# Optimization experiments

Measured on AMD Instinct MI355X. Metric: run time of the kernel, lower is better.

## Reference

```python
import jax, jax.numpy as jnp
import numpy as np

EPS = 1e-7  # keras.backend.epsilon()


def setup_inputs() -> dict:
    key = jax.random.key(0)
    kx, kw, ku = jax.random.split(key, 3)
    B, S, F = 16, 4096, 512
    x = jax.random.normal(kx, (B, S, F), dtype=jnp.float32)
    # glorot-uniform-scaled weights
    limW = np.sqrt(6.0 / (F + F)).astype(np.float32)
    W = jax.random.uniform(kw, (F, F), dtype=jnp.float32, minval=-limW, maxval=limW)
    b = jnp.zeros((F,), dtype=jnp.float32)
    limu = np.sqrt(6.0 / (F + 1)).astype(np.float32)
    u = jax.random.uniform(ku, (F,), dtype=jnp.float32, minval=-limu, maxval=limu)
    return {"x": x, "W": W, "b": b, "u": u}


def reference(x, W, b, u):
    # x: [B,S,F]  W: [F,F]  b: [F]  u: [F]
    h = jnp.tanh(jnp.einsum('bsf,fg->bsg', x, W) + b)   # [B,S,F]
    scores = jnp.einsum('bsf,f->bs', h, u)              # [B,S]
    e = jnp.exp(scores)
    # NOTE: faithful to the source, normalization is GLOBAL over all B*S scores
    a = e / (jnp.sum(e) + EPS)                          # [B,S]
    out = jnp.einsum('bsf,bs->bf', x, a)                # [B,F] weighted-sum pool over steps
    return out
```

## Files before the change

### kernel.cpp

```cpp
#include <hip/hip_runtime.h>
#include <stdint.h>

#define EPSV 1e-7f
#define FDIM 512
#define BK 64
#define NROWS 65536

typedef __bf16 bf16_t;
typedef bf16_t bf16x8 __attribute__((ext_vector_type(8)));
typedef unsigned short ushort8 __attribute__((ext_vector_type(8)));
typedef float f32x4 __attribute__((ext_vector_type(4)));

#define AS1 __attribute__((address_space(1)))
#define AS3 __attribute__((address_space(3)))

__device__ __forceinline__ unsigned short f2bf(float f) {
  union { float f; unsigned int u; } c; c.f = f;
  unsigned int u = c.u;
  unsigned int r = u + 0x7fffu + ((u >> 16) & 1u);
  return (unsigned short)(r >> 16);
}
__device__ __forceinline__ float bf2f(unsigned short s) {
  union { unsigned int u; float f; } c; c.u = ((unsigned int)s) << 16;
  return c.f;
}

__device__ __forceinline__ float fast_tanh(float x) {
  x = fminf(15.0f, fmaxf(-15.0f, x));
  float t = __expf(2.0f * x);
  return 1.0f - 2.0f * __builtin_amdgcn_rcpf(t + 1.0f);
}

__global__ __launch_bounds__(256) void convert_fused(
    const float* __restrict__ x, unsigned short* __restrict__ xbf,
    const float* __restrict__ W, unsigned short* __restrict__ Wt,
    float* __restrict__ sumE) {
  __shared__ unsigned short tile[32][34];
  const int t = threadIdx.x;
  if (blockIdx.x < 16384) {
    size_t i = ((size_t)blockIdx.x * 256 + t) * 8;
    float4 lo = *(const float4*)(x + i);
    float4 hi = *(const float4*)(x + i + 4);
    ushort8 v;
    v[0] = f2bf(lo.x); v[1] = f2bf(lo.y); v[2] = f2bf(lo.z); v[3] = f2bf(lo.w);
    v[4] = f2bf(hi.x); v[5] = f2bf(hi.y); v[6] = f2bf(hi.z); v[7] = f2bf(hi.w);
    *(ushort8*)(xbf + i) = v;
  } else {
    const int bi = blockIdx.x - 16384;
    if (bi == 0 && t == 0) *sumE = 0.0f;
    const int tx = t & 31, ty = t >> 5;
    const int bn = bi & 15, bk = bi >> 4;
    const int k0 = bk * 32, n0 = bn * 32;
#pragma unroll
    for (int i = 0; i < 4; ++i) {
      int r = ty + i * 8;
      tile[r][tx] = f2bf(W[(size_t)(k0 + r) * FDIM + n0 + tx]);
    }
    __syncthreads();
#pragma unroll
    for (int i = 0; i < 4; ++i) {
      int r = ty + i * 8;
      Wt[(size_t)(n0 + r) * FDIM + k0 + tx] = tile[tx][r];
    }
  }
}

__global__ __launch_bounds__(256, 4) void gemm_score_st(
    const unsigned short* __restrict__ xbf,
    const unsigned short* __restrict__ Wt,
    const float* __restrict__ bvec, const float* __restrict__ uvec,
    float* __restrict__ spart) {
  __shared__ unsigned short sA[128 * BK];
  __shared__ unsigned short sB[128 * BK];
  __shared__ float score_s[128];
  __shared__ float ub_s[128], bb_s[128];

  const int t = threadIdx.x;
  const int lane = t & 63;
  const int w = t >> 6;
  const int wm = w & 1;
  const int wn = w >> 1;
  const int quad = lane >> 4;
  const int l15 = lane & 15;
  const int nch = blockIdx.x >> 9;
  const int rt = blockIdx.x & 511;
  const int m0 = rt * 128;
  const int col0 = nch * 128;

  if (t < 128) {
    score_s[t] = 0.0f;
    ub_s[t] = uvec[col0 + t];
    bb_s[t] = bvec[col0 + t];
  }

  f32x4 acc[4][4];
#pragma unroll
  for (int mi = 0; mi < 4; ++mi)
#pragma unroll
    for (int ni = 0; ni < 4; ++ni) acc[mi][ni] = (f32x4){0.f, 0.f, 0.f, 0.f};

  for (int kc = 0; kc < FDIM / BK; ++kc) {
    const int kbase = kc * BK;
#pragma unroll
    for (int i = 0; i < 4; ++i) {
      int rb = w * 32 + i * 8;
      int rl = rb + (lane >> 3);
      int j = (lane & 7) ^ (rl & 7);
      const unsigned short* g = xbf + (size_t)(m0 + rl) * FDIM + kbase + j * 8;
      unsigned short* l = (unsigned short*)(sA + rb * 64);
      __builtin_amdgcn_global_load_lds((AS1 void*)(g), (AS3 void*)(l), 16, 0, 0);
    }
#pragma unroll
    for (int i = 0; i < 4; ++i) {
      int nb = w * 32 + i * 8;
      int nl = nb + (lane >> 3);
      int j = (lane & 7) ^ (nl & 7);
      const unsigned short* g = Wt + (size_t)(col0 + nl) * FDIM + kbase + j * 8;
      unsigned short* l = (unsigned short*)(sB + nb * 64);
      __builtin_amdgcn_global_load_lds((AS1 void*)(g), (AS3 void*)(l), 16, 0, 0);
    }
    __syncthreads();
#pragma unroll
    for (int ks = 0; ks < 2; ++ks) {
      bf16x8 af[4], bfr[4];
#pragma unroll
      for (int mi = 0; mi < 4; ++mi) {
        int row = wm * 64 + mi * 16 + l15;
        int phys = (ks * 4 + quad) ^ (row & 7);
        af[mi] = *(const bf16x8*)(const void*)(sA + row * 64 + phys * 8);
      }
#pragma unroll
      for (int ni = 0; ni < 4; ++ni) {
        int row = wn * 64 + ni * 16 + l15;
        int phys = (ks * 4 + quad) ^ (row & 7);
        bfr[ni] = *(const bf16x8*)(const void*)(sB + row * 64 + phys * 8);
      }
#pragma unroll
      for (int mi = 0; mi < 4; ++mi)
#pragma unroll
        for (int ni = 0; ni < 4; ++ni)
          acc[mi][ni] = __builtin_amdgcn_mfma_f32_16x16x32_bf16(
              af[mi], bfr[ni], acc[mi][ni], 0, 0, 0);
    }
    __syncthreads();
  }

  float sc[4][4];
#pragma unroll
  for (int mi = 0; mi < 4; ++mi)
#pragma unroll
    for (int r = 0; r < 4; ++r) sc[mi][r] = 0.0f;
#pragma unroll
  for (int ni = 0; ni < 4; ++ni) {
    int cl = wn * 64 + ni * 16 + l15;
    float uu = ub_s[cl], bb = bb_s[cl];
#pragma unroll
    for (int mi = 0; mi < 4; ++mi)
#pragma unroll
      for (int r = 0; r < 4; ++r)
        sc[mi][r] += uu * fast_tanh(acc[mi][ni][r] + bb);
  }
#pragma unroll
  for (int mi = 0; mi < 4; ++mi)
#pragma unroll
    for (int r = 0; r < 4; ++r) {
      float v = sc[mi][r];
      v += __shfl_xor(v, 1); v += __shfl_xor(v, 2);
      v += __shfl_xor(v, 4); v += __shfl_xor(v, 8);
      if (l15 == 0)
        atomicAdd(&score_s[wm * 64 + mi * 16 + quad * 4 + r], v);
    }
  __syncthreads();
  if (t < 128) spart[(size_t)nch * NROWS + m0 + t] = score_s[t];
}

__global__ __launch_bounds__(256, 8) void pool_score(
    const unsigned short* __restrict__ xbf, const float* __restrict__ spart,
    float* __restrict__ sumE, float* __restrict__ ppool) {
  __shared__ float e_s[32];
  __shared__ float red[4][FDIM];
  const int t = threadIdx.x;
  const int c8 = t & 63, rg = t >> 6;
  const int r0 = blockIdx.x * 32;
  if (t < 32) {
    int i = r0 + t;
    float s = spart[i] + spart[i + NROWS] + spart[i + 2 * NROWS] + spart[i + 3 * NROWS];
    float e = __expf(s);
    e_s[t] = e;
    float v = e;
    v += __shfl_xor(v, 1); v += __shfl_xor(v, 2); v += __shfl_xor(v, 4);
    v += __shfl_xor(v, 8); v += __shfl_xor(v, 16);
    if (t == 0) atomicAdd(sumE, v);
  }
  __syncthreads();
  float a[8];
#pragma unroll
  for (int j = 0; j < 8; ++j) a[j] = 0.0f;
  for (int it = 0; it < 8; ++it) {
    int row = rg * 8 + it;
    ushort8 v = *(const ushort8*)(xbf + (size_t)(r0 + row) * FDIM + c8 * 8);
    float wg = e_s[row];
#pragma unroll
    for (int j = 0; j < 8; ++j) a[j] += bf2f(v[j]) * wg;
  }
  *(float4*)&red[rg][c8 * 8]     = (float4){a[0], a[1], a[2], a[3]};
  *(float4*)&red[rg][c8 * 8 + 4] = (float4){a[4], a[5], a[6], a[7]};
  __syncthreads();
  int c = t, c2 = t + 256;
  float s0 = red[0][c] + red[1][c] + red[2][c] + red[3][c];
  float s1 = red[0][c2] + red[1][c2] + red[2][c2] + red[3][c2];
  ppool[(size_t)blockIdx.x * FDIM + c]  = s0;
  ppool[(size_t)blockIdx.x * FDIM + c2] = s1;
}

__global__ __launch_bounds__(256) void pool_reduce(
    const float* __restrict__ ppool, const float* __restrict__ sumE,
    float* __restrict__ out) {
  const int i = blockIdx.x * 256 + threadIdx.x;
  const int b = i >> 9, f = i & 511;
  float s = 0.0f;
  const float* p = ppool + (size_t)b * 128 * FDIM + f;
  for (int c = 0; c < 128; ++c) s += p[(size_t)c * FDIM];
  out[i] = s / (*sumE + EPSV);
}

__global__ void convert_W_f(const float* __restrict__ W, unsigned short* __restrict__ Wt) {
  __shared__ unsigned short tile[32][34];
  const int t = threadIdx.x;
  const int tx = t & 31, ty = t >> 5;
  const int bn = blockIdx.x & 15, bk = blockIdx.x >> 4;
  const int k0 = bk * 32, n0 = bn * 32;
#pragma unroll
  for (int i = 0; i < 4; ++i) {
    int r = ty + i * 8;
    tile[r][tx] = f2bf(W[(size_t)(k0 + r) * FDIM + n0 + tx]);
  }
  __syncthreads();
#pragma unroll
  for (int i = 0; i < 4; ++i) {
    int r = ty + i * 8;
    Wt[(size_t)(n0 + r) * FDIM + k0 + tx] = tile[tx][r];
  }
}

__global__ __launch_bounds__(256, 4) void gemm_score_f32(
    const float* __restrict__ x, const unsigned short* __restrict__ Wt,
    const float* __restrict__ bvec, const float* __restrict__ uvec,
    float* __restrict__ spart) {
  __shared__ unsigned short sA[128 * BK];
  __shared__ unsigned short sB[128 * BK];
  __shared__ float score_s[128];
  __shared__ float ub_s[128], bb_s[128];
  const int t = threadIdx.x;
  const int lane = t & 63;
  const int w = t >> 6;
  const int wm = w & 1, wn = w >> 1;
  const int quad = lane >> 4, l15 = lane & 15;
  const int nch = blockIdx.x >> 9;
  const int rt = blockIdx.x & 511;
  const int m0 = rt * 128, col0 = nch * 128;
  if (t < 128) { score_s[t] = 0.0f; ub_s[t] = uvec[col0 + t]; bb_s[t] = bvec[col0 + t]; }
  f32x4 acc[4][4];
#pragma unroll
  for (int mi = 0; mi < 4; ++mi)
#pragma unroll
    for (int ni = 0; ni < 4; ++ni) acc[mi][ni] = (f32x4){0.f, 0.f, 0.f, 0.f};
  for (int kc = 0; kc < FDIM / BK; ++kc) {
    const int kbase = kc * BK;
#pragma unroll
    for (int p = 0; p < 4; ++p) {
      int slot = t + 256 * p;
      int row = slot >> 3;
      int j = (slot & 7) ^ (row & 7);
      const float* g = x + (size_t)(m0 + row) * FDIM + kbase + j * 8;
      float4 lo = *(const float4*)g;
      float4 hi = *(const float4*)(g + 4);
      ushort8 v;
      v[0] = f2bf(lo.x); v[1] = f2bf(lo.y); v[2] = f2bf(lo.z); v[3] = f2bf(lo.w);
      v[4] = f2bf(hi.x); v[5] = f2bf(hi.y); v[6] = f2bf(hi.z); v[7] = f2bf(hi.w);
      *(ushort8*)(void*)(sA + slot * 8) = v;
    }
#pragma unroll
    for (int i = 0; i < 4; ++i) {
      int nb = w * 32 + i * 8;
      int nl = nb + (lane >> 3);
      int j = (lane & 7) ^ (nl & 7);
      const unsigned short* g = Wt + (size_t)(col0 + nl) * FDIM + kbase + j * 8;
      unsigned short* l = (unsigned short*)(sB + nb * 64);
      __builtin_amdgcn_global_load_lds((AS1 void*)(g), (AS3 void*)(l), 16, 0, 0);
    }
    __syncthreads();
#pragma unroll
    for (int ks = 0; ks < 2; ++ks) {
      bf16x8 af[4], bfr[4];
#pragma unroll
      for (int mi = 0; mi < 4; ++mi) {
        int row = wm * 64 + mi * 16 + l15;
        int phys = (ks * 4 + quad) ^ (row & 7);
        af[mi] = *(const bf16x8*)(const void*)(sA + row * 64 + phys * 8);
      }
#pragma unroll
      for (int ni = 0; ni < 4; ++ni) {
        int row = wn * 64 + ni * 16 + l15;
        int phys = (ks * 4 + quad) ^ (row & 7);
        bfr[ni] = *(const bf16x8*)(const void*)(sB + row * 64 + phys * 8);
      }
#pragma unroll
      for (int mi = 0; mi < 4; ++mi)
#pragma unroll
        for (int ni = 0; ni < 4; ++ni)
          acc[mi][ni] = __builtin_amdgcn_mfma_f32_16x16x32_bf16(
              af[mi], bfr[ni], acc[mi][ni], 0, 0, 0);
    }
    __syncthreads();
  }
  float sc[4][4];
#pragma unroll
  for (int mi = 0; mi < 4; ++mi)
#pragma unroll
    for (int r = 0; r < 4; ++r) sc[mi][r] = 0.0f;
#pragma unroll
  for (int ni = 0; ni < 4; ++ni) {
    int cl = wn * 64 + ni * 16 + l15;
    float uu = ub_s[cl], bb = bb_s[cl];
#pragma unroll
    for (int mi = 0; mi < 4; ++mi)
#pragma unroll
      for (int r = 0; r < 4; ++r)
        sc[mi][r] += uu * fast_tanh(acc[mi][ni][r] + bb);
  }
#pragma unroll
  for (int mi = 0; mi < 4; ++mi)
#pragma unroll
    for (int r = 0; r < 4; ++r) {
      float v = sc[mi][r];
      v += __shfl_xor(v, 1); v += __shfl_xor(v, 2);
      v += __shfl_xor(v, 4); v += __shfl_xor(v, 8);
      if (l15 == 0)
        atomicAdd(&score_s[wm * 64 + mi * 16 + quad * 4 + r], v);
    }
  __syncthreads();
  if (t < 128) spart[(size_t)nch * NROWS + m0 + t] = score_s[t];
}

__global__ void score_exp(float* __restrict__ spart, float* __restrict__ sumE) {
  __shared__ float ws_[4];
  const int t = threadIdx.x;
  const int i = blockIdx.x * 256 + t;
  float s = spart[i] + spart[i + NROWS] + spart[i + 2 * NROWS] + spart[i + 3 * NROWS];
  float e = __expf(s);
  spart[i] = e;
  float v = e;
  v += __shfl_xor(v, 1);  v += __shfl_xor(v, 2);  v += __shfl_xor(v, 4);
  v += __shfl_xor(v, 8);  v += __shfl_xor(v, 16); v += __shfl_xor(v, 32);
  if ((t & 63) == 0) ws_[t >> 6] = v;
  __syncthreads();
  if (t == 0) atomicAdd(sumE, ws_[0] + ws_[1] + ws_[2] + ws_[3]);
}

__global__ __launch_bounds__(256) void pool_k(
    const float* __restrict__ x, const float* __restrict__ e,
    const float* __restrict__ sumE, float* __restrict__ out) {
  __shared__ float e_s[128];
  __shared__ float4 red[128];
  const int t = threadIdx.x;
  const int b = blockIdx.x >> 5, chunk = blockIdx.x & 31;
  const int g0 = b * 4096 + chunk * 128;
  if (t < 128) e_s[t] = e[g0 + t];
  __syncthreads();
  const int parity = t >> 7, f4 = t & 127;
  float ax = 0.f, ay = 0.f, az = 0.f, aw = 0.f;
  for (int r = 0; r < 64; ++r) {
    int row = r * 2 + parity;
    const float4 xv = *(const float4*)(x + (size_t)(g0 + row) * FDIM + f4 * 4);
    float wgt = e_s[row];
    ax += xv.x * wgt; ay += xv.y * wgt; az += xv.z * wgt; aw += xv.w * wgt;
  }
  if (parity) red[f4] = (float4){ax, ay, az, aw};
  __syncthreads();
  if (!parity) {
    float4 o = red[f4];
    float inv = 1.0f / (*sumE + EPSV);
    float* op = out + (size_t)b * FDIM + f4 * 4;
    atomicAdd(op + 0, (ax + o.x) * inv);
    atomicAdd(op + 1, (ay + o.y) * inv);
    atomicAdd(op + 2, (az + o.z) * inv);
    atomicAdd(op + 3, (aw + o.w) * inv);
  }
}

extern "C" void kernel_launch(void* const* d_in, const int* in_sizes, int n_in,
                              void* d_out, int out_size, void* d_ws, size_t ws_size,
                              hipStream_t stream) {
  (void)in_sizes; (void)n_in;
  const float* x = (const float*)d_in[0];
  const float* W = (const float*)d_in[1];
  const float* b = (const float*)d_in[2];
  const float* u = (const float*)d_in[3];
  float* out = (float*)d_out;

  char* p = (char*)d_ws;
  unsigned short* Wt = (unsigned short*)p;            p += (size_t)FDIM * FDIM * 2;
  float* spart = (float*)p;                           p += (size_t)4 * NROWS * 4;
  float* sumE = (float*)p;                            p += 256;
  float* ppool = (float*)p;                           p += (size_t)2048 * FDIM * 4;
  unsigned short* xbf = (unsigned short*)p;           p += (size_t)NROWS * FDIM * 2;
  const size_t need = (size_t)(p - (char*)d_ws);
  const bool big = ws_size >= need;

  if (big) {
    convert_fused<<<dim3(16384 + 256), dim3(256), 0, stream>>>(x, xbf, W, Wt, sumE);
    gemm_score_st<<<dim3(2048), dim3(256), 0, stream>>>(xbf, Wt, b, u, spart);
    pool_score<<<dim3(2048), dim3(256), 0, stream>>>(xbf, spart, sumE, ppool);
    pool_reduce<<<dim3(32), dim3(256), 0, stream>>>(ppool, sumE, out);
  } else {
    hipMemsetAsync(sumE, 0, sizeof(float), stream);
    hipMemsetAsync(d_out, 0, (size_t)out_size * sizeof(float), stream);
    convert_W_f<<<dim3(256), dim3(256), 0, stream>>>(W, Wt);
    gemm_score_f32<<<dim3(2048), dim3(256), 0, stream>>>(x, Wt, b, u, spart);
    score_exp<<<dim3(NROWS / 256), dim3(256), 0, stream>>>(spart, sumE);
    pool_k<<<dim3(512), dim3(256), 0, stream>>>(x, spart, sumE, out);
  }
}
```

Measured before the change: 284.0 us.

## Fuse score exp and weighted pooling into GEMM tail via last-block counter

Removes the separate pool_score kernel. Each GEMM block increments a per-row-tile atomic counter, and the last of the four column-chunk blocks combines the partial scores, applies exp, adds to the global sum, and pools its 128 rows of bf16 x into a per-tile partial. This saves a kernel launch and a pass that re-reads spart, and it reads x while that tile may still be in cache. In exchange it adds threadfences, an atomic per block, a memset of the counters, and serial tail work on one block in four.

```diff
diff --git a/kernel.cpp b/kernel.cpp
--- a/kernel.cpp
+++ b/kernel.cpp
@@ -23,6 +23,9 @@
 __device__ __forceinline__ float bf2f(unsigned short s) {
   union { unsigned int u; float f; } c; c.u = ((unsigned int)s) << 16;
   return c.f;
+}
+__device__ __forceinline__ float asfloat_u(unsigned int u) {
+  union { unsigned int u; float f; } c; c.u = u; return c.f;
 }
 
 __device__ __forceinline__ float fast_tanh(float x) {
@@ -69,11 +72,14 @@
     const unsigned short* __restrict__ xbf,
     const unsigned short* __restrict__ Wt,
     const float* __restrict__ bvec, const float* __restrict__ uvec,
-    float* __restrict__ spart) {
+    float* __restrict__ spart, unsigned int* __restrict__ cnt,
+    float* __restrict__ sumE, float* __restrict__ ppool) {
   __shared__ unsigned short sA[128 * BK];
   __shared__ unsigned short sB[128 * BK];
   __shared__ float score_s[128];
   __shared__ float ub_s[128], bb_s[128];
+  __shared__ float wsum[2];
+  __shared__ int flag_s;
 
   const int t = threadIdx.x;
   const int lane = t & 63;
@@ -172,45 +178,38 @@
     }
   __syncthreads();
   if (t < 128) spart[(size_t)nch * NROWS + m0 + t] = score_s[t];
-}
-
-__global__ __launch_bounds__(256, 8) void pool_score(
-    const unsigned short* __restrict__ xbf, const float* __restrict__ spart,
-    float* __restrict__ sumE, float* __restrict__ ppool) {
-  __shared__ float e_s[32];
-  __shared__ float red[4][FDIM];
-  const int t = threadIdx.x;
-  const int c8 = t & 63, rg = t >> 6;
-  const int r0 = blockIdx.x * 32;
-  if (t < 32) {
-    int i = r0 + t;
-    float s = spart[i] + spart[i + NROWS] + spart[i + 2 * NROWS] + spart[i + 3 * NROWS];
+
+  __threadfence();
+  __syncthreads();
+  if (t == 0) flag_s = (atomicAdd(&cnt[rt], 1u) == 3u);
+  __syncthreads();
+  if (!flag_s) return;
+  __threadfence();
+
+  if (t < 128) {
+    size_t base = m0 + t;
+    float s = spart[base] + spart[NROWS + base] +
+              spart[2 * NROWS + base] + spart[3 * NROWS + base];
     float e = __expf(s);
-    e_s[t] = e;
+    score_s[t] = e;
     float v = e;
-    v += __shfl_xor(v, 1); v += __shfl_xor(v, 2); v += __shfl_xor(v, 4);
-    v += __shfl_xor(v, 8); v += __shfl_xor(v, 16);
-    if (t == 0) atomicAdd(sumE, v);
-  }
-  __syncthreads();
-  float a[8];
-#pragma unroll
-  for (int j = 0; j < 8; ++j) a[j] = 0.0f;
-  for (int it = 0; it < 8; ++it) {
-    int row = rg * 8 + it;
-    ushort8 v = *(const ushort8*)(xbf + (size_t)(r0 + row) * FDIM + c8 * 8);
-    float wg = e_s[row];
-#pragma unroll
-    for (int j = 0; j < 8; ++j) a[j] += bf2f(v[j]) * wg;
-  }
-  *(float4*)&red[rg][c8 * 8]     = (float4){a[0], a[1], a[2], a[3]};
-  *(float4*)&red[rg][c8 * 8 + 4] = (float4){a[4], a[5], a[6], a[7]};
-  __syncthreads();
-  int c = t, c2 = t + 256;
-  float s0 = red[0][c] + red[1][c] + red[2][c] + red[3][c];
-  float s1 = red[0][c2] + red[1][c2] + red[2][c2] + red[3][c2];
-  ppool[(size_t)blockIdx.x * FDIM + c]  = s0;
-  ppool[(size_t)blockIdx.x * FDIM + c2] = s1;
+    v += __shfl_xor(v, 1);  v += __shfl_xor(v, 2);  v += __shfl_xor(v, 4);
+    v += __shfl_xor(v, 8);  v += __shfl_xor(v, 16); v += __shfl_xor(v, 32);
+    if (lane == 0) wsum[t >> 6] = v;
+  }
+  __syncthreads();
+  if (t == 0) atomicAdd(sumE, wsum[0] + wsum[1]);
+
+  float a0 = 0.f, a1 = 0.f;
+  const unsigned short* xb = xbf + (size_t)m0 * FDIM + t * 2;
+#pragma unroll 8
+  for (int r = 0; r < 128; ++r) {
+    unsigned int pv = *(const unsigned int*)(xb + (size_t)r * FDIM);
+    float wg = score_s[r];
+    a0 += asfloat_u(pv << 16) * wg;
+    a1 += asfloat_u(pv & 0xffff0000u) * wg;
+  }
+  *(float2*)(ppool + (size_t)rt * FDIM + t * 2) = (float2){a0, a1};
 }
 
 __global__ __launch_bounds__(256) void pool_reduce(
@@ -219,8 +218,9 @@
   const int i = blockIdx.x * 256 + threadIdx.x;
   const int b = i >> 9, f = i & 511;
   float s = 0.0f;
-  const float* p = ppool + (size_t)b * 128 * FDIM + f;
-  for (int c = 0; c < 128; ++c) s += p[(size_t)c * FDIM];
+  const float* p = ppool + (size_t)b * 32 * FDIM + f;
+#pragma unroll
+  for (int c = 0; c < 32; ++c) s += p[(size_t)c * FDIM];
   out[i] = s / (*sumE + EPSV);
 }
 
@@ -403,15 +403,17 @@
   unsigned short* Wt = (unsigned short*)p;            p += (size_t)FDIM * FDIM * 2;
   float* spart = (float*)p;                           p += (size_t)4 * NROWS * 4;
   float* sumE = (float*)p;                            p += 256;
-  float* ppool = (float*)p;                           p += (size_t)2048 * FDIM * 4;
+  unsigned int* cnt = (unsigned int*)p;               p += 512 * 4 + 256;
+  float* ppool = (float*)p;                           p += (size_t)512 * FDIM * 4;
   unsigned short* xbf = (unsigned short*)p;           p += (size_t)NROWS * FDIM * 2;
   const size_t need = (size_t)(p - (char*)d_ws);
   const bool big = ws_size >= need;
 
   if (big) {
+    hipMemsetAsync(cnt, 0, 512 * sizeof(unsigned int), stream);
     convert_fused<<<dim3(16384 + 256), dim3(256), 0, stream>>>(x, xbf, W, Wt, sumE);
-    gemm_score_st<<<dim3(2048), dim3(256), 0, stream>>>(xbf, Wt, b, u, spart);
-    pool_score<<<dim3(2048), dim3(256), 0, stream>>>(xbf, spart, sumE, ppool);
+    gemm_score_st<<<dim3(2048), dim3(256), 0, stream>>>(xbf, Wt, b, u, spart,
+                                                        cnt, sumE, ppool);
     pool_reduce<<<dim3(32), dim3(256), 0, stream>>>(ppool, sumE, out);
   } else {
     hipMemsetAsync(sumE, 0, sizeof(float), stream);
```

Measured after the change: 448.7 us. 58.0% more time.

## Double-buffer LDS tiles in bf16 GEMM-score kernel with K=32 stages

Applied to the files above, without the earlier changes.

Replaces the single-buffered K=64 tile loop in the GEMM+score kernel with a two-stage LDS ping-pong of K=32 tiles. The global-to-LDS load for the next stage is issued before computing on the current one, and only one barrier is needed per iteration. This is meant to hide global load latency behind MFMA work. LDS use stays the same, but there are twice as many iterations, each with a single MFMA k-step. The swizzle changes to a 4-way XOR, which may affect bank conflicts. There is also no explicit vmcnt wait before the barrier, so correctness depends on the compiler inserting one.

```diff
diff --git a/kernel.cpp b/kernel.cpp
--- a/kernel.cpp
+++ b/kernel.cpp
@@ -3,7 +3,6 @@
 
 #define EPSV 1e-7f
 #define FDIM 512
-#define BK 64
 #define NROWS 65536
 
 typedef __bf16 bf16_t;
@@ -65,13 +64,13 @@
   }
 }
 
-__global__ __launch_bounds__(256, 4) void gemm_score_st(
+__global__ __launch_bounds__(256, 4) void gemm_score_db(
     const unsigned short* __restrict__ xbf,
     const unsigned short* __restrict__ Wt,
     const float* __restrict__ bvec, const float* __restrict__ uvec,
     float* __restrict__ spart) {
-  __shared__ unsigned short sA[128 * BK];
-  __shared__ unsigned short sB[128 * BK];
+  __shared__ unsigned short sA[2][128 * 32];
+  __shared__ unsigned short sB[2][128 * 32];
   __shared__ float score_s[128];
   __shared__ float ub_s[128], bb_s[128];
 
@@ -93,57 +92,62 @@
     bb_s[t] = bvec[col0 + t];
   }
 
+  const unsigned short* abase = xbf + (size_t)m0 * FDIM;
+  const unsigned short* bbase = Wt + (size_t)col0 * FDIM;
+
+#define STAGE2(SRC, SMEM, KC, BUF)                                          \
+  {                                                                         \
+    const int kbase_ = (KC)*32;                                             \
+    _Pragma("unroll") for (int i_ = 0; i_ < 2; ++i_) {                      \
+      int idx_ = w * 2 + i_;                                                \
+      int slot_ = idx_ * 64 + lane;                                         \
+      int r_ = slot_ >> 2;                                                  \
+      int kb_ = (slot_ & 3) ^ (r_ & 3);                                     \
+      const unsigned short* g_ = SRC + (size_t)r_ * FDIM + kbase_ + kb_ * 8;\
+      unsigned short* l_ = (unsigned short*)(&SMEM[BUF][idx_ * 512]);       \
+      __builtin_amdgcn_global_load_lds((AS1 void*)(g_), (AS3 void*)(l_),    \
+                                       16, 0, 0);                           \
+    }                                                                       \
+  }
+
   f32x4 acc[4][4];
 #pragma unroll
   for (int mi = 0; mi < 4; ++mi)
 #pragma unroll
     for (int ni = 0; ni < 4; ++ni) acc[mi][ni] = (f32x4){0.f, 0.f, 0.f, 0.f};
 
-  for (int kc = 0; kc < FDIM / BK; ++kc) {
-    const int kbase = kc * BK;
-#pragma unroll
-    for (int i = 0; i < 4; ++i) {
-      int rb = w * 32 + i * 8;
-      int rl = rb + (lane >> 3);
-      int j = (lane & 7) ^ (rl & 7);
-      const unsigned short* g = xbf + (size_t)(m0 + rl) * FDIM + kbase + j * 8;
-      unsigned short* l = (unsigned short*)(sA + rb * 64);
-      __builtin_amdgcn_global_load_lds((AS1 void*)(g), (AS3 void*)(l), 16, 0, 0);
-    }
-#pragma unroll
-    for (int i = 0; i < 4; ++i) {
-      int nb = w * 32 + i * 8;
-      int nl = nb + (lane >> 3);
-      int j = (lane & 7) ^ (nl & 7);
-      const unsigned short* g = Wt + (size_t)(col0 + nl) * FDIM + kbase + j * 8;
-      unsigned short* l = (unsigned short*)(sB + nb * 64);
-      __builtin_amdgcn_global_load_lds((AS1 void*)(g), (AS3 void*)(l), 16, 0, 0);
-    }
+  STAGE2(abase, sA, 0, 0)
+  STAGE2(bbase, sB, 0, 0)
+
+#pragma unroll
+  for (int kc = 0; kc < 16; ++kc) {
+    const int cur = kc & 1, nxt = cur ^ 1;
     __syncthreads();
-#pragma unroll
-    for (int ks = 0; ks < 2; ++ks) {
-      bf16x8 af[4], bfr[4];
-#pragma unroll
-      for (int mi = 0; mi < 4; ++mi) {
-        int row = wm * 64 + mi * 16 + l15;
-        int phys = (ks * 4 + quad) ^ (row & 7);
-        af[mi] = *(const bf16x8*)(const void*)(sA + row * 64 + phys * 8);
-      }
-#pragma unroll
-      for (int ni = 0; ni < 4; ++ni) {
-        int row = wn * 64 + ni * 16 + l15;
-        int phys = (ks * 4 + quad) ^ (row & 7);
-        bfr[ni] = *(const bf16x8*)(const void*)(sB + row * 64 + phys * 8);
-      }
-#pragma unroll
-      for (int mi = 0; mi < 4; ++mi)
-#pragma unroll
-        for (int ni = 0; ni < 4; ++ni)
-          acc[mi][ni] = __builtin_amdgcn_mfma_f32_16x16x32_bf16(
-              af[mi], bfr[ni], acc[mi][ni], 0, 0, 0);
-    }
-    __syncthreads();
-  }
+    if (kc < 15) {
+      STAGE2(abase, sA, kc + 1, nxt)
+      STAGE2(bbase, sB, kc + 1, nxt)
+    }
+    bf16x8 af[4], bfr[4];
+#pragma unroll
+    for (int mi = 0; mi < 4; ++mi) {
+      int r = wm * 64 + mi * 16 + l15;
+      int p = quad ^ (r & 3);
+      af[mi] = *(const bf16x8*)(const void*)(&sA[cur][r * 32 + p * 8]);
+    }
+#pragma unroll
+    for (int ni = 0; ni < 4; ++ni) {
+      int r = wn * 64 + ni * 16 + l15;
+      int p = quad ^ (r & 3);
+      bfr[ni] = *(const bf16x8*)(const void*)(&sB[cur][r * 32 + p * 8]);
+    }
+#pragma unroll
+    for (int mi = 0; mi < 4; ++mi)
+#pragma unroll
+      for (int ni = 0; ni < 4; ++ni)
+        acc[mi][ni] = __builtin_amdgcn_mfma_f32_16x16x32_bf16(
+            af[mi], bfr[ni], acc[mi][ni], 0, 0, 0);
+  }
+#undef STAGE2
 
   float sc[4][4];
 #pragma unroll
@@ -247,8 +251,8 @@
     const float* __restrict__ x, const unsigned short* __restrict__ Wt,
     const float* __restrict__ bvec, const float* __restrict__ uvec,
     float* __restrict__ spart) {
-  __shared__ unsigned short sA[128 * BK];
-  __shared__ unsigned short sB[128 * BK];
+  __shared__ unsigned short sA[128 * 64];
+  __shared__ unsigned short sB[128 * 64];
   __shared__ float score_s[128];
   __shared__ float ub_s[128], bb_s[128];
   const int t = threadIdx.x;
@@ -265,8 +269,8 @@
   for (int mi = 0; mi < 4; ++mi)
 #pragma unroll
     for (int ni = 0; ni < 4; ++ni) acc[mi][ni] = (f32x4){0.f, 0.f, 0.f, 0.f};
-  for (int kc = 0; kc < FDIM / BK; ++kc) {
-    const int kbase = kc * BK;
+  for (int kc = 0; kc < 8; ++kc) {
+    const int kbase = kc * 64;
 #pragma unroll
     for (int p = 0; p < 4; ++p) {
       int slot = t + 256 * p;
@@ -410,7 +414,7 @@
 
   if (big) {
     convert_fused<<<dim3(16384 + 256), dim3(256), 0, stream>>>(x, xbf, W, Wt, sumE);
-    gemm_score_st<<<dim3(2048), dim3(256), 0, stream>>>(xbf, Wt, b, u, spart);
+    gemm_score_db<<<dim3(2048), dim3(256), 0, stream>>>(xbf, Wt, b, u, spart);
     pool_score<<<dim3(2048), dim3(256), 0, stream>>>(xbf, spart, sumE, ppool);
     pool_reduce<<<dim3(32), dim3(256), 0, stream>>>(ppool, sumE, out);
   } else {
```

New measurement: 291.3 us. 2.6% more time.
